# Kernel optimization log

Measured on AMD Instinct MI355X. Metric: run time of the kernel, lower is better.

Reference implementation:

```python
import jax, jax.numpy as jnp
import numpy as np

BS, C_IN, L = 64, 64, 4096
C_OUT, KS, K, RATIO = 128, 7, 4, 4
HIDDEN = C_IN // RATIO
PAD, TEMP = 3, 30.0


def setup_inputs() -> dict:
    key = jax.random.key(0)
    k1, k2, k3, k4, k5 = jax.random.split(key, 5)
    x = jax.random.normal(k1, (BS, C_IN, L), dtype=jnp.float32)
    # attention 1x1 convs stored as matmul matrices
    w_attn1 = jax.random.normal(k2, (HIDDEN, C_IN), dtype=jnp.float32) * (2.0 / C_IN) ** 0.5
    w_attn2 = jax.random.normal(k3, (K, HIDDEN), dtype=jnp.float32) * (2.0 / HIDDEN) ** 0.5
    # K-bank conv weights [K, out, in, ks] and biases [K, out]
    weight = jax.random.normal(k4, (K, C_OUT, C_IN, KS), dtype=jnp.float32) * 0.05
    bias = jax.random.normal(k5, (K, C_OUT), dtype=jnp.float32) * 0.05
    return {"x": x, "w_attn1": w_attn1, "w_attn2": w_attn2, "weight": weight, "bias": bias}


def reference(x, w_attn1, w_attn2, weight, bias):
    # Attention1d: global avg pool -> 1x1 conv -> relu -> 1x1 conv -> softmax(./T)
    pooled = jnp.mean(x, axis=-1)                      # [bs, C_in]
    h = jax.nn.relu(pooled @ w_attn1.T)                # [bs, hidden]
    logits = h @ w_attn2.T                             # [bs, K]
    att = jax.nn.softmax(logits / TEMP, axis=-1)       # [bs, K]

    # softmax-weighted aggregation of the K weight banks -> per-sample kernels
    agg_w = jnp.einsum('bk,koif->boif', att, weight)   # [bs, out, in, ks]
    agg_b = att @ bias                                 # [bs, out]

    # per-sample conv1d (the grouped-conv trick), vectorized with vmap
    def conv_one(xi, wi):
        # xi: [C_in, L], wi: [out, in, ks]
        return jax.lax.conv_general_dilated(
            xi[None], wi, window_strides=(1,), padding=[(PAD, PAD)],
            dimension_numbers=('NCH', 'OIH', 'NCH'))[0]  # [out, L]

    out = jax.vmap(conv_one)(x, agg_w) + agg_b[:, :, None]  # [bs, out, L]
    return out
```

## Files before the change

### kernel.cpp

```cpp
#include <hip/hip_runtime.h>

typedef __bf16 bf16;
typedef __bf16 bf16x8 __attribute__((ext_vector_type(8)));
typedef __bf16 bf16x2 __attribute__((ext_vector_type(2)));
typedef float f32x4 __attribute__((ext_vector_type(4)));

#define BS 64
#define CI 64
#define LEN 4096
#define CO 128
#define KS 7
#define NK 4
#define HID 16
#define TEMP 30.0f

#define KTOT 448
#define WROW 456
#define WBAT (CO * WROW)
#define XROW 72
#define XC 134
#define LTILE 128
#define TPB 4
#define WST 68

__global__ void pool_kernel(const float* __restrict__ x, float* __restrict__ pooled) {
    int bc = blockIdx.x;
    const float4* xp = (const float4*)(x + (size_t)bc * LEN);
    int t = threadIdx.x;
    float s = 0.f;
#pragma unroll
    for (int j = 0; j < 4; ++j) {
        float4 v = xp[t + 256 * j];
        s += (v.x + v.y) + (v.z + v.w);
    }
#pragma unroll
    for (int off = 32; off > 0; off >>= 1) s += __shfl_down(s, off, 64);
    __shared__ float red[4];
    if ((t & 63) == 0) red[t >> 6] = s;
    __syncthreads();
    if (t == 0) pooled[bc] = (red[0] + red[1] + red[2] + red[3]) * (1.0f / LEN);
}

__global__ void attn_kernel(const float* __restrict__ pooled,
                            const float* __restrict__ w1,
                            const float* __restrict__ w2,
                            const float* __restrict__ bias,
                            float* __restrict__ att_g,
                            float* __restrict__ aggb_g) {
    int b = blockIdx.x, t = threadIdx.x;
    __shared__ float p[CI], h[HID], att[NK];
    if (t < CI) p[t] = pooled[b * CI + t];
    __syncthreads();
    if (t < HID) {
        float s = 0.f;
        for (int i = 0; i < CI; ++i) s += p[i] * w1[t * CI + i];
        h[t] = fmaxf(s, 0.f);
    }
    __syncthreads();
    if (t == 0) {
        float lg[NK];
        float m = -1e30f;
        for (int k = 0; k < NK; ++k) {
            float s = 0.f;
            for (int j = 0; j < HID; ++j) s += h[j] * w2[k * HID + j];
            lg[k] = s * (1.0f / TEMP);
            m = fmaxf(m, lg[k]);
        }
        float e[NK], tot = 0.f;
        for (int k = 0; k < NK; ++k) { e[k] = expf(lg[k] - m); tot += e[k]; }
        float inv = 1.0f / tot;
        for (int k = 0; k < NK; ++k) { att[k] = e[k] * inv; att_g[b * NK + k] = att[k]; }
    }
    __syncthreads();
    if (t < CO) {
        float s = 0.f;
        for (int k = 0; k < NK; ++k) s += att[k] * bias[k * CO + t];
        aggb_g[b * CO + t] = s;
    }
}

__global__ void aggw_kernel(const float* __restrict__ weight,
                            const float* __restrict__ att_g,
                            bf16* __restrict__ wagg) {
    int o = blockIdx.x >> 1;
    int bh = blockIdx.x & 1;
    int t = threadIdx.x;
    __shared__ float lw[4 * KTOT];
    __shared__ __align__(16) float attl[128];

    const float* wo = weight + o * KTOT;
    for (int idx = t; idx < 4 * KTOT; idx += 256) {
        int bank = idx / KTOT;
        int r = idx - bank * KTOT;
        lw[idx] = wo[(size_t)bank * (CO * KTOT) + r];
    }
    if (t < 128) attl[t] = att_g[bh * 128 + t];
    __syncthreads();

    if (t < 224) {
        float w8[8];
#pragma unroll
        for (int j = 0; j < 2; ++j) {
            int kout = 2 * t + j;
            int i = kout & 63, f = kout >> 6;
#pragma unroll
            for (int bank = 0; bank < 4; ++bank)
                w8[j * 4 + bank] = lw[bank * KTOT + i * KS + f];
        }
        for (int bb = 0; bb < 32; ++bb) {
            int b = bh * 32 + bb;
            float4 a = *(const float4*)&attl[bb * 4];
            float v0 = a.x * w8[0] + a.y * w8[1] + a.z * w8[2] + a.w * w8[3];
            float v1 = a.x * w8[4] + a.y * w8[5] + a.z * w8[6] + a.w * w8[7];
            bf16x2 pk; pk[0] = (bf16)v0; pk[1] = (bf16)v1;
            *(bf16x2*)(wagg + (size_t)b * WBAT + o * WROW + 2 * t) = pk;
        }
    }
}

struct XStage { float4 m[8]; float e1, e2; };

__global__ __launch_bounds__(256, 2) void conv_kernel(
    const float* __restrict__ x,
    const bf16* __restrict__ wagg,
    const float* __restrict__ aggb,
    float* __restrict__ out) {
    __shared__ __align__(16) bf16 lds_x[2][XC * XROW];
    __shared__ __align__(16) float lds_st[4][32 * WST];

    int nwg = gridDim.x;
    int bid = blockIdx.x;
    int logical = (bid & 7) * (nwg >> 3) + (bid >> 3);
    int b = logical >> 4;
    int rem = logical & 15;
    int oh = rem >> 3, lsp = rem & 7;

    int t = threadIdx.x;
    int lane = t & 63, wid = t >> 6;
    int ln = lane & 15, g = lane >> 4;
    int wm = wid >> 1, wn = wid & 1;

    const bf16* wgb = wagg + (size_t)b * WBAT
                    + (size_t)(oh * 64 + wm * 32 + ln) * WROW + g * 8;
    bf16x8 av[2][14];
#pragma unroll
    for (int mf = 0; mf < 2; ++mf)
#pragma unroll
        for (int kk = 0; kk < 14; ++kk)
            av[mf][kk] = *(const bf16x8*)(wgb + mf * 16 * WROW + kk * 32);

    int l0base = lsp * (LTILE * TPB);
    int si = t >> 2, sf = t & 3;
    const float* xb = x + (size_t)b * CI * LEN;

    auto load_x = [&](int l0, XStage& s) {
#pragma unroll
        for (int j = 0; j < 8; ++j) {
            int c4 = sf + 4 * j;
            s.m[j] = *(const float4*)(xb + (size_t)si * LEN + l0 + 4 * c4);
        }
        int i1 = t / 6, s1 = t - i1 * 6;
        int c1 = (s1 < 3) ? s1 : (128 + s1);
        int gl1 = l0 - 3 + c1;
        s.e1 = (gl1 >= 0 && gl1 < LEN) ? xb[(size_t)i1 * LEN + gl1] : 0.f;
        s.e2 = 0.f;
        if (t < 128) {
            int e2 = 256 + t, i2 = e2 / 6, s2 = e2 - i2 * 6;
            int c2 = (s2 < 3) ? s2 : (128 + s2);
            int gl2 = l0 - 3 + c2;
            s.e2 = (gl2 >= 0 && gl2 < LEN) ? xb[(size_t)i2 * LEN + gl2] : 0.f;
        }
    };
    auto write_x = [&](int buf, const XStage& s) {
        bf16* lb = lds_x[buf];
#pragma unroll
        for (int j = 0; j < 8; ++j) {
            int c4 = sf + 4 * j;
#pragma unroll
            for (int dl = 0; dl < 4; ++dl) {
                float v = (&s.m[j].x)[dl];
                lb[(4 * c4 + 3 + dl) * XROW + si] = (bf16)v;
            }
        }
        int i1 = t / 6, s1 = t - i1 * 6;
        int c1 = (s1 < 3) ? s1 : (128 + s1);
        lb[c1 * XROW + i1] = (bf16)s.e1;
        if (t < 128) {
            int e2 = 256 + t, i2 = e2 / 6, s2 = e2 - i2 * 6;
            int c2 = (s2 < 3) ? s2 : (128 + s2);
            lb[c2 * XROW + i2] = (bf16)s.e2;
        }
    };

    float bias_r[2][4];
#pragma unroll
    for (int mf = 0; mf < 2; ++mf)
#pragma unroll
        for (int r = 0; r < 4; ++r)
            bias_r[mf][r] = aggb[b * CO + oh * 64 + wm * 32 + mf * 16 + g * 4 + r];

    XStage s0;
    load_x(l0base, s0);
    write_x(0, s0);
    __syncthreads();

    float* st = &lds_st[wid][0];
    size_t orow0 = ((size_t)(b * CO + oh * 64 + wm * 32)) * LEN;

    for (int tl = 0; tl < TPB; ++tl) {
        int l0 = l0base + tl * LTILE;
        XStage sn;
        if (tl + 1 < TPB) load_x(l0 + LTILE, sn);

        f32x4 acc[2][4];
#pragma unroll
        for (int mf = 0; mf < 2; ++mf)
#pragma unroll
            for (int nf = 0; nf < 4; ++nf)
                acc[mf][nf] = (f32x4){0.f, 0.f, 0.f, 0.f};

        const bf16* bp = lds_x[tl & 1] + (wn * 64 + ln) * XROW + g * 8;

#pragma unroll
        for (int kk = 0; kk < 14; ++kk) {
            int boff = (kk >> 1) * XROW + (kk & 1) * 32;
            bf16x8 bv[4];
#pragma unroll
            for (int nf = 0; nf < 4; ++nf)
                bv[nf] = *(const bf16x8*)(bp + nf * 16 * XROW + boff);
#pragma unroll
            for (int mf = 0; mf < 2; ++mf)
#pragma unroll
                for (int nf = 0; nf < 4; ++nf)
                    acc[mf][nf] = __builtin_amdgcn_mfma_f32_16x16x32_bf16(
                        av[mf][kk], bv[nf], acc[mf][nf], 0, 0, 0);
        }

#pragma unroll
        for (int mf = 0; mf < 2; ++mf)
#pragma unroll
            for (int nf = 0; nf < 4; ++nf)
#pragma unroll
                for (int r = 0; r < 4; ++r)
                    st[(mf * 16 + g * 4 + r) * WST + nf * 16 + ln] =
                        acc[mf][nf][r] + bias_r[mf][r];
        asm volatile("s_waitcnt lgkmcnt(0)" ::: "memory");
        __builtin_amdgcn_sched_barrier(0);
#pragma unroll
        for (int s = 0; s < 8; ++s) {
            int rl = s * 4 + g;
            f32x4 v = *(const f32x4*)(st + rl * WST + 4 * ln);
            *(f32x4*)(out + orow0 + (size_t)rl * LEN + l0 + wn * 64 + 4 * ln) = v;
        }

        if (tl + 1 < TPB) write_x((tl + 1) & 1, sn);
        if (tl + 1 < TPB) __syncthreads();
    }
}

extern "C" void kernel_launch(void* const* d_in, const int* in_sizes, int n_in,
                              void* d_out, int out_size, void* d_ws, size_t ws_size,
                              hipStream_t stream) {
    const float* x  = (const float*)d_in[0];
    const float* w1 = (const float*)d_in[1];
    const float* w2 = (const float*)d_in[2];
    const float* wt = (const float*)d_in[3];
    const float* bs = (const float*)d_in[4];
    float* out = (float*)d_out;

    bf16* wagg = (bf16*)d_ws;
    float* pooled = (float*)((char*)d_ws + (size_t)BS * WBAT * 2);
    float* att_g  = pooled + BS * CI;
    float* aggb   = att_g + BS * NK;

    pool_kernel<<<BS * CI, 256, 0, stream>>>(x, pooled);
    attn_kernel<<<BS, 256, 0, stream>>>(pooled, w1, w2, bs, att_g, aggb);
    aggw_kernel<<<CO * 2, 256, 0, stream>>>(wt, att_g, wagg);
    conv_kernel<<<BS * 16, 256, 0, stream>>>(x, wagg, aggb, out);
}
```

Before: 68.43 us.

## Store conv outputs directly from accumulators and double tiles per block

Removes the per-wave LDS staging buffer used to transpose accumulators into coalesced float4 output rows, writing each accumulator element straight to global memory instead. Also doubles the number of length tiles processed per workgroup and halves the grid, amortizing the per-block weight register loads. This cuts LDS traffic and synchronization but produces narrower, less coalesced global stores and fewer blocks for load balance.

```diff
diff --git a/kernel.cpp b/kernel.cpp
--- a/kernel.cpp
+++ b/kernel.cpp
@@ -20,8 +20,7 @@
 #define XROW 72
 #define XC 134
 #define LTILE 128
-#define TPB 4
-#define WST 68
+#define TPB 8
 
 __global__ void pool_kernel(const float* __restrict__ x, float* __restrict__ pooled) {
     int bc = blockIdx.x;
@@ -126,14 +125,13 @@
     const float* __restrict__ aggb,
     float* __restrict__ out) {
     __shared__ __align__(16) bf16 lds_x[2][XC * XROW];
-    __shared__ __align__(16) float lds_st[4][32 * WST];
 
     int nwg = gridDim.x;
     int bid = blockIdx.x;
     int logical = (bid & 7) * (nwg >> 3) + (bid >> 3);
-    int b = logical >> 4;
-    int rem = logical & 15;
-    int oh = rem >> 3, lsp = rem & 7;
+    int b = logical >> 3;
+    int rem = logical & 7;
+    int oh = rem >> 2, lsp = rem & 3;
 
     int t = threadIdx.x;
     int lane = t & 63, wid = t >> 6;
@@ -193,19 +191,20 @@
     };
 
     float bias_r[2][4];
+    int orow_off[2][4];
 #pragma unroll
     for (int mf = 0; mf < 2; ++mf)
 #pragma unroll
-        for (int r = 0; r < 4; ++r)
-            bias_r[mf][r] = aggb[b * CO + oh * 64 + wm * 32 + mf * 16 + g * 4 + r];
+        for (int r = 0; r < 4; ++r) {
+            int o = oh * 64 + wm * 32 + mf * 16 + g * 4 + r;
+            bias_r[mf][r] = aggb[b * CO + o];
+            orow_off[mf][r] = (b * CO + o) * LEN;
+        }
 
     XStage s0;
     load_x(l0base, s0);
     write_x(0, s0);
     __syncthreads();
-
-    float* st = &lds_st[wid][0];
-    size_t orow0 = ((size_t)(b * CO + oh * 64 + wm * 32)) * LEN;
 
     for (int tl = 0; tl < TPB; ++tl) {
         int l0 = l0base + tl * LTILE;
@@ -239,22 +238,17 @@
 #pragma unroll
         for (int mf = 0; mf < 2; ++mf)
 #pragma unroll
-            for (int nf = 0; nf < 4; ++nf)
+            for (int nf = 0; nf < 4; ++nf) {
+                int l = l0 + wn * 64 + nf * 16 + ln;
 #pragma unroll
                 for (int r = 0; r < 4; ++r)
-                    st[(mf * 16 + g * 4 + r) * WST + nf * 16 + ln] =
-                        acc[mf][nf][r] + bias_r[mf][r];
-        asm volatile("s_waitcnt lgkmcnt(0)" ::: "memory");
-        __builtin_amdgcn_sched_barrier(0);
-#pragma unroll
-        for (int s = 0; s < 8; ++s) {
-            int rl = s * 4 + g;
-            f32x4 v = *(const f32x4*)(st + rl * WST + 4 * ln);
-            *(f32x4*)(out + orow0 + (size_t)rl * LEN + l0 + wn * 64 + 4 * ln) = v;
-        }
-
-        if (tl + 1 < TPB) write_x((tl + 1) & 1, sn);
-        if (tl + 1 < TPB) __syncthreads();
+                    out[(size_t)orow_off[mf][r] + l] = acc[mf][nf][r] + bias_r[mf][r];
+            }
+
+        if (tl + 1 < TPB) {
+            write_x((tl + 1) & 1, sn);
+            __syncthreads();
+        }
     }
 }
 
@@ -276,5 +270,5 @@
     pool_kernel<<<BS * CI, 256, 0, stream>>>(x, pooled);
     attn_kernel<<<BS, 256, 0, stream>>>(pooled, w1, w2, bs, att_g, aggb);
     aggw_kernel<<<CO * 2, 256, 0, stream>>>(wt, att_g, wagg);
-    conv_kernel<<<BS * 16, 256, 0, stream>>>(x, wagg, aggb, out);
-}
+    conv_kernel<<<BS * 8, 256, 0, stream>>>(x, wagg, aggb, out);
+}
```

New measurement: 64.99 us. -5.0%, faster.
